# Kernel tuning notes

Hardware: AMD Instinct MI355X
Metric: run time of the kernel (lower is better)

The kernel has to match this reference:

```python
import jax, jax.numpy as jnp
import numpy as np


def _compute_features(ff):
    # ff: (..., 4) = [rx, ry, rvx, rvy]
    rx, ry, rvx, rvy = ff[..., 0], ff[..., 1], ff[..., 2], ff[..., 3]
    dist_sq = rx * rx + ry * ry
    dist = jnp.sqrt(dist_sq + 1e-06)
    inv_dist = 1.0 / (dist + 0.1)
    dir_x = rx / (dist + 1e-06)
    dir_y = ry / (dist + 1e-06)
    speed_sq = rvx * rvx + rvy * rvy
    rel_speed = jnp.sqrt(speed_sq + 1e-06)
    dot_vp = rvx * rx + rvy * ry
    closing_speed = dot_vp / (dist + 1e-06)
    ttca = jnp.tanh(-dot_vp / (speed_sq + 1e-06))
    return jnp.stack(
        [rx, ry, rvx, rvy, dist, inv_dist, rel_speed, closing_speed,
         dir_x, dir_y, ttca, dot_vp], axis=-1)  # (..., 12)


def setup_inputs() -> dict:
    key = jax.random.key(0)
    k0, k1, k2, k3, k4 = jax.random.split(key, 5)
    B, N, H, HID, IN = 16, 256, 8, 64, 12
    ff = jax.random.normal(k0, (B, N, N, 4), dtype=jnp.float32)
    # nn.Linear default init scale ~ 1/sqrt(fan_in); use small random weights
    W1 = jax.random.normal(k1, (IN, HID), dtype=jnp.float32) / np.sqrt(IN)
    b1 = jax.random.normal(k2, (HID,), dtype=jnp.float32) / np.sqrt(IN)
    W2 = jax.random.normal(k3, (HID, H), dtype=jnp.float32) / np.sqrt(HID)
    b2 = jax.random.normal(k4, (H,), dtype=jnp.float32) / np.sqrt(HID)
    return {"fundamental_features": ff, "W1": W1, "b1": b1, "W2": W2, "b2": b2}


def reference(fundamental_features, W1, b1, W2, b2):
    feats = _compute_features(fundamental_features)          # (B, N, N, 12)
    h = jax.nn.silu(jnp.einsum('bnmf,fh->bnmh', feats, W1) + b1)  # (B, N, N, 64)
    bias = jnp.einsum('bnmh,ho->bnmo', h, W2) + b2            # (B, N, N, H)
    return jnp.transpose(bias, (0, 3, 1, 2))                  # (B, H, N, N)
```

## Files before the change

### kernel.cpp

```cpp
#include <hip/hip_runtime.h>
#include <hip/hip_bf16.h>

#define NH 8
#define HID 64
#define NPAIRS (16 * 256 * 256)
#define BLOCK 256
#define LROWD 36

typedef __attribute__((ext_vector_type(8))) short bf16x8;
typedef __attribute__((ext_vector_type(4))) float f32x4;
typedef __attribute__((ext_vector_type(16))) float f32x16;

union F8 { bf16x8 v; unsigned u[4]; uint4 q4; };

__device__ inline unsigned pk2(float a, float b) {
    __hip_bfloat162 h = __float22bfloat162_rn(make_float2(a, b));
    unsigned u;
    __builtin_memcpy(&u, &h, 4);
    return u;
}

__device__ inline int Hperm(int j) { return (j & 1) * 32 + (j >> 1); }

__global__ void pack_weights(const float* __restrict__ W1, const float* __restrict__ b1,
                             const float* __restrict__ W2, const float* __restrict__ b2,
                             unsigned char* __restrict__ ws) {
    int l = threadIdx.x;
    int n32 = l & 31, q2 = l >> 5;
    int n16 = l & 15, q4 = l >> 4;
    unsigned* B1 = (unsigned*)ws;
    unsigned* B2 = (unsigned*)(ws + 2048);
    float* b2v = (float*)(ws + 4096);
    for (int m = 0; m < 2; ++m) {
        int h = m * 32 + n32;
        for (int j2 = 0; j2 < 4; ++j2) {
            int k0 = q2 * 8 + 2 * j2, k1 = k0 + 1;
            float v0 = (k0 < 12) ? W1[k0 * HID + h] : (k0 == 12 ? b1[h] : 0.f);
            float v1 = (k1 < 12) ? W1[k1 * HID + h] : 0.f;
            B1[(m * 64 + l) * 4 + j2] = pk2(v0, v1);
        }
    }
    for (int kc = 0; kc < 2; ++kc)
        for (int j2 = 0; j2 < 4; ++j2) {
            int k0 = kc * 32 + q4 * 8 + 2 * j2;
            float v0 = (n16 < NH) ? W2[Hperm(k0) * NH + n16] : 0.f;
            float v1 = (n16 < NH) ? W2[Hperm(k0 + 1) * NH + n16] : 0.f;
            B2[(kc * 64 + l) * 4 + j2] = pk2(v0, v1);
        }
    b2v[l] = (n16 < NH) ? b2[n16] : 0.f;
}

__global__ __launch_bounds__(BLOCK) void relfeat_mfma4(
    const float* __restrict__ ff, const unsigned char* __restrict__ ws,
    float* __restrict__ out)
{
    __shared__ unsigned lds[4][32 * LROWD];
    const int tid = threadIdx.x;
    const int w = tid >> 6, l = tid & 63;
    const int n32 = l & 31, q2 = l >> 5;
    const int n16 = l & 15, q4 = l >> 4;
    unsigned* my = lds[w];

    F8 B1f[2], B2f[2];
    B1f[0].q4 = ((const uint4*)ws)[l];
    B1f[1].q4 = ((const uint4*)ws)[64 + l];
    B2f[0].q4 = ((const uint4*)(ws + 2048))[l];
    B2f[1].q4 = ((const uint4*)(ws + 2048))[64 + l];
    const float b2s = ((const float*)(ws + 4096))[l];

    f32x16 z16;
    #pragma unroll
    for (int r = 0; r < 16; ++r) z16[r] = 0.f;

    const int wave_base = (blockIdx.x * 4 + w) * 128;

    #pragma unroll
    for (int it = 0; it < 2; ++it) {
        const int pbase = wave_base + it * 64;

        float4 v = ((const float4*)ff)[pbase + l];
        float rx = v.x, ry = v.y, rvx = v.z, rvy = v.w;
        float dist_sq = rx * rx + ry * ry;
        float invd = __builtin_amdgcn_rsqf(dist_sq + 1e-6f);
        float dist = (dist_sq + 1e-6f) * invd;
        float speed_sq = rvx * rvx + rvy * rvy;
        float dot_vp = rvx * rx + rvy * ry;
        float inv_dist = __builtin_amdgcn_rcpf(dist + 0.1f);
        float rel_speed = sqrtf(speed_sq + 1e-6f);
        float closing = dot_vp * invd;
        float dir_x = rx * invd, dir_y = ry * invd;
        float zz = -dot_vp * __builtin_amdgcn_rcpf(speed_sq + 1e-6f);
        float ez = __expf(2.f * zz);
        float ttca = 1.f - 2.f * __builtin_amdgcn_rcpf(ez + 1.f);

        unsigned c0 = pk2(rx, ry), c1 = pk2(rvx, rvy);
        unsigned c2 = pk2(dist, inv_dist), c3 = pk2(rel_speed, closing);
        unsigned c4 = pk2(dir_x, dir_y), c5 = pk2(ttca, dot_vp);
        unsigned sw0 = (unsigned)__shfl_xor((int)c0, 32);
        unsigned sw1 = (unsigned)__shfl_xor((int)c1, 32);
        unsigned sw2 = (unsigned)__shfl_xor((int)c2, 32);
        unsigned sw3 = (unsigned)__shfl_xor((int)c3, 32);
        unsigned sw4 = (unsigned)__shfl_xor((int)c4, 32);
        unsigned sw5 = (unsigned)__shfl_xor((int)c5, 32);

        const bool hi = (q2 != 0);
        F8 frag[2];
        frag[0].u[0] = hi ? sw4 : c0;
        frag[0].u[1] = hi ? sw5 : c1;
        frag[0].u[2] = hi ? 0x00003f80u : c2;
        frag[0].u[3] = hi ? 0u : c3;
        frag[1].u[0] = hi ? c4 : sw0;
        frag[1].u[1] = hi ? c5 : sw1;
        frag[1].u[2] = hi ? 0x00003f80u : sw2;
        frag[1].u[3] = hi ? 0u : sw3;

        #pragma unroll
        for (int G = 0; G < 2; ++G) {
            const int pg = pbase + G * 32;

            f32x16 d1a = __builtin_amdgcn_mfma_f32_32x32x16_bf16(frag[G].v, B1f[0].v, z16, 0, 0, 0);
            f32x16 d1b = __builtin_amdgcn_mfma_f32_32x32x16_bf16(frag[G].v, B1f[1].v, z16, 0, 0, 0);

            #pragma unroll
            for (int r = 0; r < 16; ++r) {
                int prow = (r & 3) + 8 * (r >> 2) + 4 * q2;
                float x0 = d1a[r], x1 = d1b[r];
                float s0 = x0 * __builtin_amdgcn_rcpf(1.f + __expf(-x0));
                float s1 = x1 * __builtin_amdgcn_rcpf(1.f + __expf(-x1));
                my[prow * LROWD + n32] = pk2(s0, s1);
            }

            #pragma unroll
            for (int hl = 0; hl < 2; ++hl) {
                f32x4 d2 = {b2s, b2s, b2s, b2s};
                #pragma unroll
                for (int kc = 0; kc < 2; ++kc) {
                    F8 a2;
                    a2.q4 = *(const uint4*)((const unsigned char*)my
                              + (hl * 16 + n16) * (LROWD * 4) + kc * 64 + q4 * 16);
                    d2 = __builtin_amdgcn_mfma_f32_16x16x32_bf16(a2.v, B2f[kc].v, d2, 0, 0, 0);
                }
                if (n16 < NH) {
                    int p0 = pg + hl * 16 + q4 * 4;
                    int b = p0 >> 16, lo16 = p0 & 65535;
                    float4 st; st.x = d2[0]; st.y = d2[1]; st.z = d2[2]; st.w = d2[3];
                    *(float4*)(out + (size_t)b * (NH * 65536) + (size_t)n16 * 65536 + lo16) = st;
                }
            }
        }
    }
}

extern "C" void kernel_launch(void* const* d_in, const int* in_sizes, int n_in,
                              void* d_out, int out_size, void* d_ws, size_t ws_size,
                              hipStream_t stream) {
    const float* ff = (const float*)d_in[0];
    const float* W1 = (const float*)d_in[1];
    const float* b1 = (const float*)d_in[2];
    const float* W2 = (const float*)d_in[3];
    const float* b2 = (const float*)d_in[4];
    float* out = (float*)d_out;
    unsigned char* ws = (unsigned char*)d_ws;

    pack_weights<<<1, 64, 0, stream>>>(W1, b1, W2, b2, ws);
    const int grid = NPAIRS / (128 * 4);
    relfeat_mfma4<<<grid, BLOCK, 0, stream>>>(ff, ws, out);
}
```

Measured before the change: 103.8 us.

## Keep hidden activations in registers by transposing MFMAs, drop LDS staging and pack kernel

The layer-1 MFMA is transposed so its output layout matches the B operand of a second 32x32x16 MFMA. SiLU outputs can then go straight into the layer-2 matmul without the LDS write/read round trip. Weights are packed per thread inside the main kernel, so the separate pack_weights launch is gone. The cost is redundant weight loading in every block, extra layer-2 MFMA work on padded rows (8 useful of 32), and scalar rather than float4 output stores.

```diff
diff --git a/kernel.cpp b/kernel.cpp
--- a/kernel.cpp
+++ b/kernel.cpp
@@ -5,10 +5,8 @@
 #define HID 64
 #define NPAIRS (16 * 256 * 256)
 #define BLOCK 256
-#define LROWD 36
 
 typedef __attribute__((ext_vector_type(8))) short bf16x8;
-typedef __attribute__((ext_vector_type(4))) float f32x4;
 typedef __attribute__((ext_vector_type(16))) float f32x16;
 
 union F8 { bf16x8 v; unsigned u[4]; uint4 q4; };
@@ -20,53 +18,45 @@
     return u;
 }
 
-__device__ inline int Hperm(int j) { return (j & 1) * 32 + (j >> 1); }
+__device__ inline int hperm(int m) {
+    return (m & 0x13) | ((m & 8) >> 1) | ((m & 4) << 1);
+}
 
-__global__ void pack_weights(const float* __restrict__ W1, const float* __restrict__ b1,
-                             const float* __restrict__ W2, const float* __restrict__ b2,
-                             unsigned char* __restrict__ ws) {
-    int l = threadIdx.x;
-    int n32 = l & 31, q2 = l >> 5;
-    int n16 = l & 15, q4 = l >> 4;
-    unsigned* B1 = (unsigned*)ws;
-    unsigned* B2 = (unsigned*)(ws + 2048);
-    float* b2v = (float*)(ws + 4096);
-    for (int m = 0; m < 2; ++m) {
-        int h = m * 32 + n32;
+__global__ __launch_bounds__(BLOCK) void relfeat_mfma6(
+    const float* __restrict__ ff, const float* __restrict__ W1,
+    const float* __restrict__ b1, const float* __restrict__ W2,
+    const float* __restrict__ b2, float* __restrict__ out)
+{
+    const int tid = threadIdx.x;
+    const int w = tid >> 6, l = tid & 63;
+    const int n32 = l & 31, q2 = l >> 5;
+
+    F8 B1f[2];
+    #pragma unroll
+    for (int mh = 0; mh < 2; ++mh) {
+        int h = 32 * mh + hperm(n32);
+        #pragma unroll
         for (int j2 = 0; j2 < 4; ++j2) {
             int k0 = q2 * 8 + 2 * j2, k1 = k0 + 1;
             float v0 = (k0 < 12) ? W1[k0 * HID + h] : (k0 == 12 ? b1[h] : 0.f);
             float v1 = (k1 < 12) ? W1[k1 * HID + h] : 0.f;
-            B1[(m * 64 + l) * 4 + j2] = pk2(v0, v1);
+            B1f[mh].u[j2] = pk2(v0, v1);
         }
     }
-    for (int kc = 0; kc < 2; ++kc)
+    F8 W2A[4];
+    #pragma unroll
+    for (int kc = 0; kc < 4; ++kc) {
+        #pragma unroll
         for (int j2 = 0; j2 < 4; ++j2) {
-            int k0 = kc * 32 + q4 * 8 + 2 * j2;
-            float v0 = (n16 < NH) ? W2[Hperm(k0) * NH + n16] : 0.f;
-            float v1 = (n16 < NH) ? W2[Hperm(k0 + 1) * NH + n16] : 0.f;
-            B2[(kc * 64 + l) * 4 + j2] = pk2(v0, v1);
+            int hid = 16 * kc + q2 * 8 + 2 * j2;
+            float v0 = (n32 < NH) ? W2[hid * NH + n32] : 0.f;
+            float v1 = (n32 < NH) ? W2[(hid + 1) * NH + n32] : 0.f;
+            W2A[kc].u[j2] = pk2(v0, v1);
         }
-    b2v[l] = (n16 < NH) ? b2[n16] : 0.f;
-}
-
-__global__ __launch_bounds__(BLOCK) void relfeat_mfma4(
-    const float* __restrict__ ff, const unsigned char* __restrict__ ws,
-    float* __restrict__ out)
-{
-    __shared__ unsigned lds[4][32 * LROWD];
-    const int tid = threadIdx.x;
-    const int w = tid >> 6, l = tid & 63;
-    const int n32 = l & 31, q2 = l >> 5;
-    const int n16 = l & 15, q4 = l >> 4;
-    unsigned* my = lds[w];
-
-    F8 B1f[2], B2f[2];
-    B1f[0].q4 = ((const uint4*)ws)[l];
-    B1f[1].q4 = ((const uint4*)ws)[64 + l];
-    B2f[0].q4 = ((const uint4*)(ws + 2048))[l];
-    B2f[1].q4 = ((const uint4*)(ws + 2048))[64 + l];
-    const float b2s = ((const float*)(ws + 4096))[l];
+    }
+    float b2r[4];
+    #pragma unroll
+    for (int r = 0; r < 4; ++r) b2r[r] = b2[r + 4 * q2];
 
     f32x16 z16;
     #pragma unroll
@@ -118,34 +108,33 @@
         for (int G = 0; G < 2; ++G) {
             const int pg = pbase + G * 32;
 
-            f32x16 d1a = __builtin_amdgcn_mfma_f32_32x32x16_bf16(frag[G].v, B1f[0].v, z16, 0, 0, 0);
-            f32x16 d1b = __builtin_amdgcn_mfma_f32_32x32x16_bf16(frag[G].v, B1f[1].v, z16, 0, 0, 0);
+            f32x16 d1a = __builtin_amdgcn_mfma_f32_32x32x16_bf16(B1f[0].v, frag[G].v, z16, 0, 0, 0);
+            f32x16 d1b = __builtin_amdgcn_mfma_f32_32x32x16_bf16(B1f[1].v, frag[G].v, z16, 0, 0, 0);
 
+            f32x16 d2 = z16;
             #pragma unroll
-            for (int r = 0; r < 16; ++r) {
-                int prow = (r & 3) + 8 * (r >> 2) + 4 * q2;
-                float x0 = d1a[r], x1 = d1b[r];
-                float s0 = x0 * __builtin_amdgcn_rcpf(1.f + __expf(-x0));
-                float s1 = x1 * __builtin_amdgcn_rcpf(1.f + __expf(-x1));
-                my[prow * LROWD + n32] = pk2(s0, s1);
+            for (int kc = 0; kc < 4; ++kc) {
+                const f32x16& d1 = (kc < 2) ? d1a : d1b;
+                const int rb = (kc & 1) * 8;
+                float s[8];
+                #pragma unroll
+                for (int j = 0; j < 8; ++j) {
+                    float x = d1[rb + j];
+                    s[j] = x * __builtin_amdgcn_rcpf(1.f + __expf(-x));
+                }
+                F8 bf;
+                bf.u[0] = pk2(s[0], s[1]);
+                bf.u[1] = pk2(s[2], s[3]);
+                bf.u[2] = pk2(s[4], s[5]);
+                bf.u[3] = pk2(s[6], s[7]);
+                d2 = __builtin_amdgcn_mfma_f32_32x32x16_bf16(W2A[kc].v, bf.v, d2, 0, 0, 0);
             }
 
+            int b = pg >> 16, lo16 = pg & 65535;
+            float* op = out + (size_t)b * (NH * 65536) + lo16 + n32;
             #pragma unroll
-            for (int hl = 0; hl < 2; ++hl) {
-                f32x4 d2 = {b2s, b2s, b2s, b2s};
-                #pragma unroll
-                for (int kc = 0; kc < 2; ++kc) {
-                    F8 a2;
-                    a2.q4 = *(const uint4*)((const unsigned char*)my
-                              + (hl * 16 + n16) * (LROWD * 4) + kc * 64 + q4 * 16);
-                    d2 = __builtin_amdgcn_mfma_f32_16x16x32_bf16(a2.v, B2f[kc].v, d2, 0, 0, 0);
-                }
-                if (n16 < NH) {
-                    int p0 = pg + hl * 16 + q4 * 4;
-                    int b = p0 >> 16, lo16 = p0 & 65535;
-                    float4 st; st.x = d2[0]; st.y = d2[1]; st.z = d2[2]; st.w = d2[3];
-                    *(float4*)(out + (size_t)b * (NH * 65536) + (size_t)n16 * 65536 + lo16) = st;
-                }
+            for (int r = 0; r < 4; ++r) {
+                op[(size_t)(r + 4 * q2) * 65536] = d2[r] + b2r[r];
             }
         }
     }
@@ -160,9 +149,7 @@
     const float* W2 = (const float*)d_in[3];
     const float* b2 = (const float*)d_in[4];
     float* out = (float*)d_out;
-    unsigned char* ws = (unsigned char*)d_ws;
 
-    pack_weights<<<1, 64, 0, stream>>>(W1, b1, W2, b2, ws);
     const int grid = NPAIRS / (128 * 4);
-    relfeat_mfma4<<<grid, BLOCK, 0, stream>>>(ff, ws, out);
+    relfeat_mfma6<<<grid, BLOCK, 0, stream>>>(ff, W1, b1, W2, b2, out);
 }
```

Result: no change. 102.6 us (-1.2%).
